# Kernel optimization log

Measured on AMD Instinct MI355X. Metric: run time of the kernel, lower is better.

## Reference

```python
import jax, jax.numpy as jnp
import numpy as np

B, T, D, H = 4, 2048, 1024, 16
Hd = D // H


def setup_inputs() -> dict:
    key = jax.random.key(0)
    ks = jax.random.split(key, 6)
    s = 1.0 / np.sqrt(D)
    return {
        "x": jax.random.normal(ks[0], (B, T, D), dtype=jnp.float32),
        "mask": jnp.zeros((B, T), dtype=bool),
        "Wq": jax.random.normal(ks[1], (D, D), dtype=jnp.float32) * s,
        "bq": jnp.zeros((D,), dtype=jnp.float32),
        "Wk": jax.random.normal(ks[2], (D, D), dtype=jnp.float32) * s,
        "bk": jnp.zeros((D,), dtype=jnp.float32),
        "Wv": jax.random.normal(ks[3], (D, D), dtype=jnp.float32) * s,
        "bv": jnp.zeros((D,), dtype=jnp.float32),
        "Wo": jax.random.normal(ks[4], (D, D), dtype=jnp.float32) * s,
        "bo": jnp.zeros((D,), dtype=jnp.float32),
    }


def reference(x, mask, Wq, bq, Wk, bk, Wv, bv, Wo, bo):
    b, t, d = x.shape
    # projections -> [B, T, H, Hd]
    Q = (x @ Wq + bq).reshape(b, t, H, Hd)
    K = (x @ Wk + bk).reshape(b, t, H, Hd)
    V = (x @ Wv + bv).reshape(b, t, H, Hd)
    scale = jnp.asarray(Hd, x.dtype) ** -0.5
    # full score matrix [B, H, Tq, Tk] (matches the naive torch impl)
    attn = jnp.einsum("bqhd,bkhd->bhqk", Q, K) * scale
    attn = jnp.where(mask[:, None, None, :], jnp.asarray(-1e9, attn.dtype), attn)
    attn = jax.nn.softmax(attn, axis=-1)
    out = jnp.einsum("bhqk,bkhd->bqhd", attn, V).reshape(b, t, d)
    return out @ Wo + bo
```

## Files before the change

### kernel.cpp

```cpp
#include <hip/hip_runtime.h>

using bf16 = __bf16;
typedef bf16 bf16x4 __attribute__((ext_vector_type(4)));
typedef bf16 bf16x8 __attribute__((ext_vector_type(8)));
typedef float f32x4 __attribute__((ext_vector_type(4)));
typedef float f32x8 __attribute__((ext_vector_type(8)));

#define MFMA16(a, b, c) __builtin_amdgcn_mfma_f32_16x16x32_bf16(a, b, c, 0, 0, 0)

constexpr int Bb = 4, Tt = 2048, Dd = 1024, Hh = 16, Hd = 64;
constexpr int Mrows = Bb * Tt;
constexpr float CEXP = 0.18033688011112042f;

__device__ __forceinline__ void gload_lds16(const bf16* g, bf16* lds_base) {
  __builtin_amdgcn_global_load_lds((const __attribute__((address_space(1))) void*)g,
                                   (__attribute__((address_space(3))) void*)lds_base,
                                   16, 0, 0);
}

__global__ void cast_f32_bf16_kernel(const float* __restrict__ in, bf16* __restrict__ out) {
  size_t i = ((size_t)blockIdx.x * 256 + threadIdx.x) * 8;
  f32x8 v = *(const f32x8*)(in + i);
  *(bf16x8*)(out + i) = __builtin_convertvector(v, bf16x8);
}

__global__ void transpose_cast_w4_kernel(const float* __restrict__ Wq, const float* __restrict__ Wk,
                                         const float* __restrict__ Wv, const float* __restrict__ Wo,
                                         bf16* __restrict__ Wt, bf16* __restrict__ Wot) {
  __shared__ alignas(16) float tile[64][68];
  const int tid = threadIdx.x;
  const int n0 = blockIdx.x * 64, k0 = blockIdx.y * 64, z = blockIdx.z;
  const float* W = (z == 0) ? Wq : (z == 1) ? Wk : (z == 2) ? Wv : Wo;
  bf16* dst = (z == 3) ? Wot : (Wt + (size_t)z * Dd * Dd);
  const float scale = (z == 0) ? CEXP : 1.0f;
#pragma unroll
  for (int it = 0; it < 4; ++it) {
    int chunk = tid + it * 256;
    int kr = chunk >> 4, c4 = chunk & 15;
    f32x4 v = *(const f32x4*)(W + (size_t)(k0 + kr) * Dd + n0 + c4 * 4);
    *(f32x4*)&tile[kr][c4 * 4] = v * scale;
  }
  __syncthreads();
#pragma unroll
  for (int it = 0; it < 2; ++it) {
    int chunk = tid + it * 256;
    int n = chunk & 63, k8 = chunk >> 6;
    bf16x8 o;
#pragma unroll
    for (int j = 0; j < 8; ++j) o[j] = (bf16)tile[k8 * 8 + j][n];
    *(bf16x8*)(dst + (size_t)(n0 + n) * Dd + k0 + k8 * 8) = o;
  }
}

__global__ void pack_bias_kernel(const float* __restrict__ bq, const float* __restrict__ bk,
                                 const float* __restrict__ bv, float* __restrict__ outb) {
  int i = blockIdx.x * 256 + threadIdx.x;
  float v = (i < 1024) ? bq[i] * CEXP : (i < 2048 ? bk[i - 1024] : bv[i - 2048]);
  outb[i] = v;
}

template <typename OutT>
__global__ __launch_bounds__(256)
void gemm_bf16_kernel(const bf16* __restrict__ A, const bf16* __restrict__ Bt,
                      const float* __restrict__ bias, OutT* __restrict__ C,
                      int M, int N, int K) {
  __shared__ alignas(16) bf16 As[128 * 64];
  __shared__ alignas(16) bf16 Bs[128 * 64];
  const int tid = threadIdx.x;
  const int lane = tid & 63, wave = tid >> 6;
  const int col = lane & 15, quad = lane >> 4;
  const int wr = (wave >> 1) * 64, wc = (wave & 1) * 64;
  const size_t m0 = (size_t)blockIdx.x * 128, n0 = (size_t)blockIdx.y * 128;
  const int srow = lane >> 3, schunk = (lane & 7) * 8;

  f32x4 acc[4][4];
#pragma unroll
  for (int i = 0; i < 4; ++i)
#pragma unroll
    for (int j = 0; j < 4; ++j)
#pragma unroll
      for (int r = 0; r < 4; ++r) acc[i][j][r] = 0.f;

  for (int k0 = 0; k0 < K; k0 += 64) {
#pragma unroll
    for (int it = 0; it < 4; ++it) {
      int rbase = it * 32 + wave * 8;
      gload_lds16(A + (m0 + rbase + srow) * (size_t)K + k0 + schunk, &As[rbase * 64]);
      gload_lds16(Bt + (n0 + rbase + srow) * (size_t)K + k0 + schunk, &Bs[rbase * 64]);
    }
    __syncthreads();
#pragma unroll
    for (int kk = 0; kk < 2; ++kk) {
      bf16x8 af[4], bfr[4];
#pragma unroll
      for (int i = 0; i < 4; ++i) af[i] = *(const bf16x8*)&As[(wr + i * 16 + col) * 64 + kk * 32 + quad * 8];
#pragma unroll
      for (int j = 0; j < 4; ++j) bfr[j] = *(const bf16x8*)&Bs[(wc + j * 16 + col) * 64 + kk * 32 + quad * 8];
#pragma unroll
      for (int i = 0; i < 4; ++i)
#pragma unroll
        for (int j = 0; j < 4; ++j) acc[i][j] = MFMA16(af[i], bfr[j], acc[i][j]);
    }
    __syncthreads();
  }
#pragma unroll
  for (int i = 0; i < 4; ++i)
#pragma unroll
    for (int j = 0; j < 4; ++j) {
      size_t row = m0 + wr + i * 16 + quad * 4;
      size_t c = n0 + wc + j * 16 + col;
      float bv = bias[c];
#pragma unroll
      for (int r = 0; r < 4; ++r) C[(row + r) * (size_t)N + c] = (OutT)(acc[i][j][r] + bv);
    }
}

__global__ void transpose_v_kernel(const bf16* __restrict__ qkv, bf16* __restrict__ vt) {
  __shared__ alignas(16) bf16 tile[64][72];
  const int tid = threadIdx.x;
  const int t0 = blockIdx.x * 64;
  const int h = blockIdx.y, b = blockIdx.z;
  const bf16* src = qkv + (size_t)(b * Tt + t0) * 3072 + 2048 + h * Hd;
#pragma unroll
  for (int it = 0; it < 2; ++it) {
    int chunk = tid + it * 256;
    int tr = chunk >> 3, d8 = chunk & 7;
    bf16x8 v = *(const bf16x8*)(src + (size_t)tr * 3072 + d8 * 8);
#pragma unroll
    for (int j = 0; j < 8; ++j) tile[d8 * 8 + j][tr] = v[j];
  }
  __syncthreads();
  bf16* dst = vt + ((size_t)(b * Hh + h) * Hd) * Tt + t0;
#pragma unroll
  for (int it = 0; it < 2; ++it) {
    int chunk = tid + it * 256;
    int d = chunk >> 3, t8 = chunk & 7;
    bf16x8 o = *(const bf16x8*)&tile[d][t8 * 8];
    *(bf16x8*)(dst + (size_t)d * Tt + t8 * 8) = o;
  }
}

__global__ __launch_bounds__(256, 2)
void flash_attn_kernel(const bf16* __restrict__ qkv, const bf16* __restrict__ vt,
                       const unsigned char* __restrict__ mask, bf16* __restrict__ ao) {
  __shared__ alignas(16) bf16 Ks[2][64 * 64];
  __shared__ alignas(16) bf16 Vs[2][64 * 64];
  __shared__ alignas(16) bf16 pbuf[4][4][16 * 64];

  const int tid = threadIdx.x;
  const int wave = tid >> 6, lane = tid & 63;
  const int col = lane & 15, quad = lane >> 4;
  const int id = blockIdx.x;
  const int hb = id & 63, qi2 = id >> 6;
  const int h = hb & 15, b = hb >> 4;
  const int qbase0 = qi2 * 256 + wave * 64;

  const bf16* Qp = qkv + (size_t)(b * Tt) * 3072 + h * Hd;
  const bf16* Kp = Qp + 1024;
  const bf16* Vp = vt + ((size_t)(b * Hh + h) * Hd) * Tt;
  const unsigned char* mp = mask + b * Tt;

  unsigned long long anym;
  {
    const unsigned long long* mq = (const unsigned long long*)mp;
    unsigned long long acc = 0;
#pragma unroll
    for (int j = 0; j < 4; ++j) acc |= mq[lane * 4 + j];
    anym = __ballot(acc != 0ull);
  }

  bf16x8 qf[4][2];
#pragma unroll
  for (int t = 0; t < 4; ++t)
#pragma unroll
    for (int kk = 0; kk < 2; ++kk)
      qf[t][kk] = *(const bf16x8*)(Qp + (size_t)(qbase0 + t * 16 + col) * 3072 + kk * 32 + quad * 8);

  const bf16* Ksrc = Kp + (size_t)lane * 3072 + wave * 16;
  const bf16* Vsrc = Vp + (size_t)lane * Tt + wave * 16;
  const int ss1 = ((2 * wave) ^ (lane & 7)) * 8;
  const int ss2 = ((2 * wave + 1) ^ (lane & 7)) * 8;
  const int srowoff = lane * 64;

  {
    bf16x8 k0 = *(const bf16x8*)Ksrc, k1 = *(const bf16x8*)(Ksrc + 8);
    bf16x8 v0 = *(const bf16x8*)Vsrc, v1 = *(const bf16x8*)(Vsrc + 8);
    *(bf16x8*)&Ks[0][srowoff + ss1] = k0;  *(bf16x8*)&Ks[0][srowoff + ss2] = k1;
    *(bf16x8*)&Vs[0][srowoff + ss1] = v0;  *(bf16x8*)&Vs[0][srowoff + ss2] = v1;
  }
  __syncthreads();

  f32x4 oacc[4][4];
  float lsum[4];
#pragma unroll
  for (int t = 0; t < 4; ++t) {
    lsum[t] = 0.f;
#pragma unroll
    for (int n = 0; n < 4; ++n)
#pragma unroll
      for (int r = 0; r < 4; ++r) oacc[t][n][r] = 0.f;
  }

  const int fslot0 = ((0 * 4 + quad) ^ (col & 7)) * 8;
  const int fslot1 = ((1 * 4 + quad) ^ (col & 7)) * 8;

  for (int i = 0; i < 32; ++i) {
    const int cur = i & 1, nxt = cur ^ 1;
    const int kb = i * 64;

    bf16x8 nk0, nk1, nv0, nv1;
    if (i < 31) {
      const bf16* ks = Ksrc + (size_t)(kb + 64) * 3072;
      const bf16* vs = Vsrc + (kb + 64);
      nk0 = *(const bf16x8*)ks;  nk1 = *(const bf16x8*)(ks + 8);
      nv0 = *(const bf16x8*)vs;  nv1 = *(const bf16x8*)(vs + 8);
    }

    bf16x8 kf[4][2], vf[4][2];
#pragma unroll
    for (int kt = 0; kt < 4; ++kt) {
      kf[kt][0] = *(const bf16x8*)&Ks[cur][(kt * 16 + col) * 64 + fslot0];
      kf[kt][1] = *(const bf16x8*)&Ks[cur][(kt * 16 + col) * 64 + fslot1];
    }
#pragma unroll
    for (int n = 0; n < 4; ++n) {
      vf[n][0] = *(const bf16x8*)&Vs[cur][(n * 16 + col) * 64 + fslot0];
      vf[n][1] = *(const bf16x8*)&Vs[cur][(n * 16 + col) * 64 + fslot1];
    }

    float rsv[4];
#pragma unroll
    for (int t = 0; t < 4; ++t) {
      f32x4 s[4];
#pragma unroll
      for (int kt = 0; kt < 4; ++kt)
#pragma unroll
        for (int r = 0; r < 4; ++r) s[kt][r] = 0.f;
#pragma unroll
      for (int kk = 0; kk < 2; ++kk)
#pragma unroll
        for (int kt = 0; kt < 4; ++kt) s[kt] = MFMA16(kf[kt][kk], qf[t][kk], s[kt]);

      if ((anym >> (2 * i)) & 3ull) {
#pragma unroll
        for (int kt = 0; kt < 4; ++kt)
#pragma unroll
          for (int r = 0; r < 4; ++r)
            if (mp[kb + kt * 16 + quad * 4 + r] != 0) s[kt][r] = -1e9f;
      }

      float rs = 0.f;
#pragma unroll
      for (int kt = 0; kt < 4; ++kt) {
        f32x4 pv;
#pragma unroll
        for (int r = 0; r < 4; ++r) {
          pv[r] = __builtin_amdgcn_exp2f(s[kt][r]);
          rs += pv[r];
        }
        bf16x4 pk = __builtin_convertvector(pv, bf16x4);
        int slot = ((2 * kt + (quad >> 1)) ^ (col & 7)) * 8 + (quad & 1) * 4;
        *(bf16x4*)&pbuf[wave][t][col * 64 + slot] = pk;
      }
      rs += __shfl_xor(rs, 16, 64);
      rs += __shfl_xor(rs, 32, 64);
      rsv[t] = rs;
    }

    __builtin_amdgcn_s_waitcnt(0xc07f);
#pragma unroll
    for (int t = 0; t < 4; ++t) {
      bf16x8 pf0 = *(const bf16x8*)&pbuf[wave][t][col * 64 + fslot0];
      bf16x8 pf1 = *(const bf16x8*)&pbuf[wave][t][col * 64 + fslot1];
#pragma unroll
      for (int n = 0; n < 4; ++n) {
        oacc[t][n] = MFMA16(vf[n][0], pf0, oacc[t][n]);
        oacc[t][n] = MFMA16(vf[n][1], pf1, oacc[t][n]);
      }
      lsum[t] += rsv[t];
    }

    if (i < 31) {
      *(bf16x8*)&Ks[nxt][srowoff + ss1] = nk0;  *(bf16x8*)&Ks[nxt][srowoff + ss2] = nk1;
      *(bf16x8*)&Vs[nxt][srowoff + ss1] = nv0;  *(bf16x8*)&Vs[nxt][srowoff + ss2] = nv1;
    }
    __syncthreads();
  }

#pragma unroll
  for (int t = 0; t < 4; ++t) {
    float rl = 1.0f / lsum[t];
    size_t q = (size_t)b * Tt + qbase0 + t * 16 + col;
#pragma unroll
    for (int n = 0; n < 4; ++n) {
      bf16x4 ov;
#pragma unroll
      for (int r = 0; r < 4; ++r) ov[r] = (bf16)(oacc[t][n][r] * rl);
      *(bf16x4*)(ao + q * Dd + h * Hd + n * 16 + quad * 4) = ov;
    }
  }
}

extern "C" void kernel_launch(void* const* d_in, const int* in_sizes, int n_in,
                              void* d_out, int out_size, void* d_ws, size_t ws_size,
                              hipStream_t stream) {
  const float* x = (const float*)d_in[0];
  const unsigned char* mask = (const unsigned char*)d_in[1];
  const float* Wq = (const float*)d_in[2];
  const float* bq = (const float*)d_in[3];
  const float* Wk = (const float*)d_in[4];
  const float* bk = (const float*)d_in[5];
  const float* Wv = (const float*)d_in[6];
  const float* bv = (const float*)d_in[7];
  const float* Wo = (const float*)d_in[8];
  const float* bo = (const float*)d_in[9];
  float* out = (float*)d_out;

  char* ws = (char*)d_ws;
  size_t off = 0;
  auto alloc = [&](size_t bytes) {
    char* p = ws + off;
    off += (bytes + 255) & ~(size_t)255;
    return p;
  };
  bf16* xb  = (bf16*)alloc((size_t)Mrows * Dd * 2);
  bf16* Wt  = (bf16*)alloc((size_t)3 * Dd * Dd * 2);
  bf16* Wot = (bf16*)alloc((size_t)Dd * Dd * 2);
  bf16* QKV = (bf16*)alloc((size_t)Mrows * 3 * Dd * 2);
  bf16* Vt  = (bf16*)alloc((size_t)Bb * Hh * Hd * Tt * 2);
  float* bqkv = (float*)alloc((size_t)3 * Dd * 4);

  cast_f32_bf16_kernel<<<Mrows * Dd / (256 * 8), 256, 0, stream>>>(x, xb);
  transpose_cast_w4_kernel<<<dim3(16, 16, 4), 256, 0, stream>>>(Wq, Wk, Wv, Wo, Wt, Wot);
  pack_bias_kernel<<<12, 256, 0, stream>>>(bq, bk, bv, bqkv);

  gemm_bf16_kernel<bf16><<<dim3(Mrows / 128, 3 * Dd / 128), 256, 0, stream>>>(
      xb, Wt, bqkv, QKV, Mrows, 3 * Dd, Dd);
  transpose_v_kernel<<<dim3(Tt / 64, Hh, Bb), 256, 0, stream>>>(QKV, Vt);

  bf16* AO = xb;
  flash_attn_kernel<<<dim3(512), 256, 0, stream>>>(QKV, Vt, mask, AO);
  gemm_bf16_kernel<float><<<dim3(Mrows / 128, Dd / 128), 256, 0, stream>>>(
      AO, Wot, bo, out, Mrows, Dd, Dd);
}
```

Baseline: 300.9 us.

## Fuse V transpose into QKV GEMM epilogue and keep P in registers

The QKV GEMM now writes Q and K into a narrower [M,2048] buffer and writes V directly in the transposed per-head layout, which removes the separate transpose_v kernel and its round trip through memory. The attention kernel swaps the MFMA operand order so the probability tile produced by the first MFMA can feed the PV MFMA straight from registers. This drops the LDS pbuf write/read and its wait, and V fragments are instead gathered with two 4-wide LDS reads. Row sums now go through a small LDS reduction buffer and the output is stored element by element. The trade-offs are a strided, uncoalesced epilogue store for V and scalar output stores.

```diff
diff --git a/kernel.cpp b/kernel.cpp
--- a/kernel.cpp
+++ b/kernel.cpp
@@ -59,10 +59,83 @@
   outb[i] = v;
 }
 
-template <typename OutT>
+__global__ __launch_bounds__(256)
+void gemm_qkv_kernel(const bf16* __restrict__ A, const bf16* __restrict__ Bt,
+                     const float* __restrict__ bias, bf16* __restrict__ QK,
+                     bf16* __restrict__ Vt) {
+  constexpr int K = Dd, N = 3 * Dd;
+  __shared__ alignas(16) bf16 As[128 * 64];
+  __shared__ alignas(16) bf16 Bs[128 * 64];
+  const int tid = threadIdx.x;
+  const int lane = tid & 63, wave = tid >> 6;
+  const int col = lane & 15, quad = lane >> 4;
+  const int wr = (wave >> 1) * 64, wc = (wave & 1) * 64;
+  const size_t m0 = (size_t)blockIdx.x * 128, n0 = (size_t)blockIdx.y * 128;
+  const int srow = lane >> 3, schunk = (lane & 7) * 8;
+
+  f32x4 acc[4][4];
+#pragma unroll
+  for (int i = 0; i < 4; ++i)
+#pragma unroll
+    for (int j = 0; j < 4; ++j)
+#pragma unroll
+      for (int r = 0; r < 4; ++r) acc[i][j][r] = 0.f;
+
+  for (int k0 = 0; k0 < K; k0 += 64) {
+#pragma unroll
+    for (int it = 0; it < 4; ++it) {
+      int rbase = it * 32 + wave * 8;
+      gload_lds16(A + (m0 + rbase + srow) * (size_t)K + k0 + schunk, &As[rbase * 64]);
+      gload_lds16(Bt + (n0 + rbase + srow) * (size_t)K + k0 + schunk, &Bs[rbase * 64]);
+    }
+    __syncthreads();
+#pragma unroll
+    for (int kk = 0; kk < 2; ++kk) {
+      bf16x8 af[4], bfr[4];
+#pragma unroll
+      for (int i = 0; i < 4; ++i) af[i] = *(const bf16x8*)&As[(wr + i * 16 + col) * 64 + kk * 32 + quad * 8];
+#pragma unroll
+      for (int j = 0; j < 4; ++j) bfr[j] = *(const bf16x8*)&Bs[(wc + j * 16 + col) * 64 + kk * 32 + quad * 8];
+#pragma unroll
+      for (int i = 0; i < 4; ++i)
+#pragma unroll
+        for (int j = 0; j < 4; ++j) acc[i][j] = MFMA16(af[i], bfr[j], acc[i][j]);
+    }
+    __syncthreads();
+  }
+
+  if (n0 < 2048) {
+#pragma unroll
+    for (int i = 0; i < 4; ++i)
+#pragma unroll
+      for (int j = 0; j < 4; ++j) {
+        size_t row = m0 + wr + i * 16 + quad * 4;
+        size_t c = n0 + wc + j * 16 + col;
+        float bv = bias[c];
+#pragma unroll
+        for (int r = 0; r < 4; ++r) QK[(row + r) * 2048 + c] = (bf16)(acc[i][j][r] + bv);
+      }
+  } else {
+#pragma unroll
+    for (int i = 0; i < 4; ++i)
+#pragma unroll
+      for (int j = 0; j < 4; ++j) {
+        size_t row = m0 + wr + i * 16 + quad * 4;
+        int c = (int)(n0 + wc + j * 16 + col);
+        float bv = bias[c];
+        int dall = c - 2048, hh = dall >> 6, dd = dall & 63;
+        int bi = (int)(row >> 11), trow = (int)(row & 2047);
+        bf16x4 pk;
+#pragma unroll
+        for (int r = 0; r < 4; ++r) pk[r] = (bf16)(acc[i][j][r] + bv);
+        *(bf16x4*)&Vt[((size_t)(bi * Hh + hh) * Hd + dd) * Tt + trow] = pk;
+      }
+  }
+}
+
 __global__ __launch_bounds__(256)
 void gemm_bf16_kernel(const bf16* __restrict__ A, const bf16* __restrict__ Bt,
-                      const float* __restrict__ bias, OutT* __restrict__ C,
+                      const float* __restrict__ bias, float* __restrict__ C,
                       int M, int N, int K) {
   __shared__ alignas(16) bf16 As[128 * 64];
   __shared__ alignas(16) bf16 Bs[128 * 64];
@@ -111,41 +184,16 @@
       size_t c = n0 + wc + j * 16 + col;
       float bv = bias[c];
 #pragma unroll
-      for (int r = 0; r < 4; ++r) C[(row + r) * (size_t)N + c] = (OutT)(acc[i][j][r] + bv);
-    }
-}
-
-__global__ void transpose_v_kernel(const bf16* __restrict__ qkv, bf16* __restrict__ vt) {
-  __shared__ alignas(16) bf16 tile[64][72];
-  const int tid = threadIdx.x;
-  const int t0 = blockIdx.x * 64;
-  const int h = blockIdx.y, b = blockIdx.z;
-  const bf16* src = qkv + (size_t)(b * Tt + t0) * 3072 + 2048 + h * Hd;
-#pragma unroll
-  for (int it = 0; it < 2; ++it) {
-    int chunk = tid + it * 256;
-    int tr = chunk >> 3, d8 = chunk & 7;
-    bf16x8 v = *(const bf16x8*)(src + (size_t)tr * 3072 + d8 * 8);
-#pragma unroll
-    for (int j = 0; j < 8; ++j) tile[d8 * 8 + j][tr] = v[j];
-  }
-  __syncthreads();
-  bf16* dst = vt + ((size_t)(b * Hh + h) * Hd) * Tt + t0;
-#pragma unroll
-  for (int it = 0; it < 2; ++it) {
-    int chunk = tid + it * 256;
-    int d = chunk >> 3, t8 = chunk & 7;
-    bf16x8 o = *(const bf16x8*)&tile[d][t8 * 8];
-    *(bf16x8*)(dst + (size_t)d * Tt + t8 * 8) = o;
-  }
+      for (int r = 0; r < 4; ++r) C[(row + r) * (size_t)N + c] = acc[i][j][r] + bv;
+    }
 }
 
 __global__ __launch_bounds__(256, 2)
-void flash_attn_kernel(const bf16* __restrict__ qkv, const bf16* __restrict__ vt,
+void flash_attn_kernel(const bf16* __restrict__ qk, const bf16* __restrict__ vt,
                        const unsigned char* __restrict__ mask, bf16* __restrict__ ao) {
   __shared__ alignas(16) bf16 Ks[2][64 * 64];
   __shared__ alignas(16) bf16 Vs[2][64 * 64];
-  __shared__ alignas(16) bf16 pbuf[4][4][16 * 64];
+  __shared__ alignas(16) float lred[4][64];
 
   const int tid = threadIdx.x;
   const int wave = tid >> 6, lane = tid & 63;
@@ -155,7 +203,7 @@
   const int h = hb & 15, b = hb >> 4;
   const int qbase0 = qi2 * 256 + wave * 64;
 
-  const bf16* Qp = qkv + (size_t)(b * Tt) * 3072 + h * Hd;
+  const bf16* Qp = qk + (size_t)(b * Tt) * 2048 + h * Hd;
   const bf16* Kp = Qp + 1024;
   const bf16* Vp = vt + ((size_t)(b * Hh + h) * Hd) * Tt;
   const unsigned char* mp = mask + b * Tt;
@@ -174,9 +222,9 @@
   for (int t = 0; t < 4; ++t)
 #pragma unroll
     for (int kk = 0; kk < 2; ++kk)
-      qf[t][kk] = *(const bf16x8*)(Qp + (size_t)(qbase0 + t * 16 + col) * 3072 + kk * 32 + quad * 8);
-
-  const bf16* Ksrc = Kp + (size_t)lane * 3072 + wave * 16;
+      qf[t][kk] = *(const bf16x8*)(Qp + (size_t)(qbase0 + t * 16 + col) * 2048 + kk * 32 + quad * 8);
+
+  const bf16* Ksrc = Kp + (size_t)lane * 2048 + wave * 16;
   const bf16* Vsrc = Vp + (size_t)lane * Tt + wave * 16;
   const int ss1 = ((2 * wave) ^ (lane & 7)) * 8;
   const int ss2 = ((2 * wave + 1) ^ (lane & 7)) * 8;
@@ -200,9 +248,12 @@
 #pragma unroll
       for (int r = 0; r < 4; ++r) oacc[t][n][r] = 0.f;
   }
+  const f32x4 zero4 = {0.f, 0.f, 0.f, 0.f};
 
   const int fslot0 = ((0 * 4 + quad) ^ (col & 7)) * 8;
   const int fslot1 = ((1 * 4 + quad) ^ (col & 7)) * 8;
+  const int voff = (quad & 1) * 4;
+  const int vc00 = ((0 * 4 + 0 * 2 + (quad >> 1)) ^ 9999, 0);
 
   for (int i = 0; i < 32; ++i) {
     const int cur = i & 1, nxt = cur ^ 1;
@@ -210,13 +261,13 @@
 
     bf16x8 nk0, nk1, nv0, nv1;
     if (i < 31) {
-      const bf16* ks = Ksrc + (size_t)(kb + 64) * 3072;
+      const bf16* ks = Ksrc + (size_t)(kb + 64) * 2048;
       const bf16* vs = Vsrc + (kb + 64);
       nk0 = *(const bf16x8*)ks;  nk1 = *(const bf16x8*)(ks + 8);
       nv0 = *(const bf16x8*)vs;  nv1 = *(const bf16x8*)(vs + 8);
     }
 
-    bf16x8 kf[4][2], vf[4][2];
+    bf16x8 kf[4][2], vfs[4][2];
 #pragma unroll
     for (int kt = 0; kt < 4; ++kt) {
       kf[kt][0] = *(const bf16x8*)&Ks[cur][(kt * 16 + col) * 64 + fslot0];
@@ -224,22 +275,23 @@
     }
 #pragma unroll
     for (int n = 0; n < 4; ++n) {
-      vf[n][0] = *(const bf16x8*)&Vs[cur][(n * 16 + col) * 64 + fslot0];
-      vf[n][1] = *(const bf16x8*)&Vs[cur][(n * 16 + col) * 64 + fslot1];
-    }
-
-    float rsv[4];
+      const int row = (n * 16 + col) * 64;
+      const int rx = col & 7;
+#pragma unroll
+      for (int kk = 0; kk < 2; ++kk) {
+        bf16x4 lo = *(const bf16x4*)&Vs[cur][row + ((kk * 4 + 0 + (quad >> 1)) ^ rx) * 8 + voff];
+        bf16x4 hi = *(const bf16x4*)&Vs[cur][row + ((kk * 4 + 2 + (quad >> 1)) ^ rx) * 8 + voff];
+        vfs[n][kk] = __builtin_shufflevector(lo, hi, 0, 1, 2, 3, 4, 5, 6, 7);
+      }
+    }
+
 #pragma unroll
     for (int t = 0; t < 4; ++t) {
       f32x4 s[4];
 #pragma unroll
-      for (int kt = 0; kt < 4; ++kt)
-#pragma unroll
-        for (int r = 0; r < 4; ++r) s[kt][r] = 0.f;
-#pragma unroll
-      for (int kk = 0; kk < 2; ++kk)
-#pragma unroll
-        for (int kt = 0; kt < 4; ++kt) s[kt] = MFMA16(kf[kt][kk], qf[t][kk], s[kt]);
+      for (int kt = 0; kt < 4; ++kt) s[kt] = MFMA16(kf[kt][0], qf[t][0], zero4);
+#pragma unroll
+      for (int kt = 0; kt < 4; ++kt) s[kt] = MFMA16(kf[kt][1], qf[t][1], s[kt]);
 
       if ((anym >> (2 * i)) & 3ull) {
 #pragma unroll
@@ -249,35 +301,29 @@
             if (mp[kb + kt * 16 + quad * 4 + r] != 0) s[kt][r] = -1e9f;
       }
 
+      f32x4 e[4];
       float rs = 0.f;
 #pragma unroll
-      for (int kt = 0; kt < 4; ++kt) {
-        f32x4 pv;
+      for (int kt = 0; kt < 4; ++kt)
 #pragma unroll
         for (int r = 0; r < 4; ++r) {
-          pv[r] = __builtin_amdgcn_exp2f(s[kt][r]);
-          rs += pv[r];
+          e[kt][r] = __builtin_amdgcn_exp2f(s[kt][r]);
+          rs += e[kt][r];
         }
-        bf16x4 pk = __builtin_convertvector(pv, bf16x4);
-        int slot = ((2 * kt + (quad >> 1)) ^ (col & 7)) * 8 + (quad & 1) * 4;
-        *(bf16x4*)&pbuf[wave][t][col * 64 + slot] = pk;
+      bf16x4 c0 = __builtin_convertvector(e[0], bf16x4);
+      bf16x4 c1 = __builtin_convertvector(e[1], bf16x4);
+      bf16x4 c2 = __builtin_convertvector(e[2], bf16x4);
+      bf16x4 c3 = __builtin_convertvector(e[3], bf16x4);
+      bf16x8 pf0 = __builtin_shufflevector(c0, c1, 0, 1, 2, 3, 4, 5, 6, 7);
+      bf16x8 pf1 = __builtin_shufflevector(c2, c3, 0, 1, 2, 3, 4, 5, 6, 7);
+#pragma unroll
+      for (int n = 0; n < 4; ++n) {
+        oacc[t][n] = MFMA16(pf0, vfs[n][0], oacc[t][n]);
+        oacc[t][n] = MFMA16(pf1, vfs[n][1], oacc[t][n]);
       }
       rs += __shfl_xor(rs, 16, 64);
       rs += __shfl_xor(rs, 32, 64);
-      rsv[t] = rs;
-    }
-
-    __builtin_amdgcn_s_waitcnt(0xc07f);
-#pragma unroll
-    for (int t = 0; t < 4; ++t) {
-      bf16x8 pf0 = *(const bf16x8*)&pbuf[wave][t][col * 64 + fslot0];
-      bf16x8 pf1 = *(const bf16x8*)&pbuf[wave][t][col * 64 + fslot1];
-#pragma unroll
-      for (int n = 0; n < 4; ++n) {
-        oacc[t][n] = MFMA16(vf[n][0], pf0, oacc[t][n]);
-        oacc[t][n] = MFMA16(vf[n][1], pf1, oacc[t][n]);
-      }
-      lsum[t] += rsv[t];
+      lsum[t] += rs;
     }
 
     if (i < 31) {
@@ -287,17 +333,24 @@
     __syncthreads();
   }
 
+  if (lane < 16) {
+#pragma unroll
+    for (int t = 0; t < 4; ++t) lred[wave][t * 16 + lane] = lsum[t];
+  }
+  __builtin_amdgcn_s_waitcnt(0xc07f);
 #pragma unroll
   for (int t = 0; t < 4; ++t) {
-    float rl = 1.0f / lsum[t];
-    size_t q = (size_t)b * Tt + qbase0 + t * 16 + col;
-#pragma unroll
-    for (int n = 0; n < 4; ++n) {
-      bf16x4 ov;
-#pragma unroll
-      for (int r = 0; r < 4; ++r) ov[r] = (bf16)(oacc[t][n][r] * rl);
-      *(bf16x4*)(ao + q * Dd + h * Hd + n * 16 + quad * 4) = ov;
-    }
+    f32x4 lv = *(const f32x4*)&lred[wave][t * 16 + quad * 4];
+    f32x4 rl;
+#pragma unroll
+    for (int r = 0; r < 4; ++r) rl[r] = __builtin_amdgcn_rcpf(lv[r]);
+#pragma unroll
+    for (int n = 0; n < 4; ++n)
+#pragma unroll
+      for (int r = 0; r < 4; ++r) {
+        size_t q = (size_t)b * Tt + qbase0 + t * 16 + quad * 4 + r;
+        ao[q * Dd + h * Hd + n * 16 + col] = (bf16)(oacc[t][n][r] * rl[r]);
+      }
   }
 }
 
@@ -326,7 +379,7 @@
   bf16* xb  = (bf16*)alloc((size_t)Mrows * Dd * 2);
   bf16* Wt  = (bf16*)alloc((size_t)3 * Dd * Dd * 2);
   bf16* Wot = (bf16*)alloc((size_t)Dd * Dd * 2);
-  bf16* QKV = (bf16*)alloc((size_t)Mrows * 3 * Dd * 2);
+  bf16* QK  = (bf16*)alloc((size_t)Mrows * 2048 * 2);
   bf16* Vt  = (bf16*)alloc((size_t)Bb * Hh * Hd * Tt * 2);
   float* bqkv = (float*)alloc((size_t)3 * Dd * 4);
 
@@ -334,12 +387,11 @@
   transpose_cast_w4_kernel<<<dim3(16, 16, 4), 256, 0, stream>>>(Wq, Wk, Wv, Wo, Wt, Wot);
   pack_bias_kernel<<<12, 256, 0, stream>>>(bq, bk, bv, bqkv);
 
-  gemm_bf16_kernel<bf16><<<dim3(Mrows / 128, 3 * Dd / 128), 256, 0, stream>>>(
-      xb, Wt, bqkv, QKV, Mrows, 3 * Dd, Dd);
-  transpose_v_kernel<<<dim3(Tt / 64, Hh, Bb), 256, 0, stream>>>(QKV, Vt);
+  gemm_qkv_kernel<<<dim3(Mrows / 128, 3 * Dd / 128), 256, 0, stream>>>(
+      xb, Wt, bqkv, QK, Vt);
 
   bf16* AO = xb;
-  flash_attn_kernel<<<dim3(512), 256, 0, stream>>>(QKV, Vt, mask, AO);
-  gemm_bf16_kernel<float><<<dim3(Mrows / 128, Dd / 128), 256, 0, stream>>>(
+  flash_attn_kernel<<<dim3(512), 256, 0, stream>>>(QK, Vt, mask, AO);
+  gemm_bf16_kernel<<<dim3(Mrows / 128, Dd / 128), 256, 0, stream>>>(
       AO, Wot, bo, out, Mrows, Dd, Dd);
 }
```

Result: faster. 291.1 us (-3.3%).
